# Optimization experiments

Hardware: AMD Instinct MI355X
Metric: run time of the kernel (lower is better)

## Reference

```python
import jax, jax.numpy as jnp
import numpy as np

NUM_EXECUTORS = 50
NUM_DAG_FEATURES = 3
EMB_DAG = 16
EMB_GLOB = 16
HIDDEN = [64, 64, 32]
B = 60000            # number of jobs (one per env in the batched rollout)
NODES_PER_JOB = 10
NODE_FEAT = 5


def _init_mlp(key, dims):
    ws, bs = [], []
    for i in range(len(dims) - 1):
        key, k = jax.random.split(key)
        scale = 1.0 / np.sqrt(dims[i])
        ws.append(jax.random.uniform(k, (dims[i], dims[i + 1]), jnp.float32, -scale, scale))
        bs.append(jnp.zeros((dims[i + 1],), jnp.float32))
    return ws, bs


def setup_inputs() -> dict:
    rng = np.random.default_rng(0)
    n_nodes = B * NODES_PER_JOB
    # dag_batch.ptr: job i owns nodes [i*NODES_PER_JOB, (i+1)*NODES_PER_JOB)
    ptr = np.arange(B + 1, dtype=np.int64) * NODES_PER_JOB
    job_indices = rng.permutation(B).astype(np.int64)
    # ragged action counts per job (exec_mask is a prefix mask of length num_exec_acts[i])
    num_exec_acts = rng.integers(1, NUM_EXECUTORS + 1, size=B).astype(np.int64)
    n_sel = num_exec_acts[job_indices]
    T = int(n_sel.sum())
    # per-ragged-row executor index: concat([arange(n) for n in n_sel]), vectorized
    starts = np.cumsum(n_sel) - n_sel
    exec_act_idx = (np.arange(T, dtype=np.int64) - np.repeat(starts, n_sel)).astype(np.int64)

    key = jax.random.key(0)
    k_x, k_hd, k_hg, k_mlp = jax.random.split(key, 4)
    x = jax.random.normal(k_x, (n_nodes, NODE_FEAT), jnp.float32)
    h_dag = jax.random.normal(k_hd, (B, EMB_DAG), jnp.float32)
    h_glob = jax.random.normal(k_hg, (B, EMB_GLOB), jnp.float32)

    in_dim = NUM_DAG_FEATURES + EMB_DAG + EMB_GLOB + 1  # 36
    ws, bs = _init_mlp(k_mlp, [in_dim] + HIDDEN + [1])

    return {
        "x": x,
        "h_dag": h_dag,
        "h_glob": h_glob,
        "ptr": jnp.asarray(ptr),
        "job_indices": jnp.asarray(job_indices),
        "num_exec_acts": jnp.asarray(num_exec_acts),
        "exec_act_idx": jnp.asarray(exec_act_idx),
        "W1": ws[0], "b1": bs[0],
        "W2": ws[1], "b2": bs[1],
        "W3": ws[2], "b3": bs[2],
        "W4": ws[3], "b4": bs[3],
    }


def reference(x, h_dag, h_glob, ptr, job_indices, num_exec_acts, exec_act_idx,
              W1, b1, W2, b2, W3, b3, W4, b4):
    T = exec_act_idx.shape[0]                       # total ragged action rows (static)
    J = job_indices.shape[0]
    # masked gather: dag features at each dag's start node, then select jobs
    x_dag = x[ptr[:-1], :NUM_DAG_FEATURES][job_indices]        # [J, 3]
    h_dag_sel = h_dag[job_indices]                              # [J, 16]
    x_h_dag = jnp.concatenate([x_dag, h_dag_sel], axis=1)       # [J, 19]
    # variable repeat_interleave -> gather by repeated row index
    n_sel = num_exec_acts[job_indices]
    rpt = jnp.repeat(jnp.arange(J), n_sel, total_repeat_length=T)
    x_h_rpt = x_h_dag[rpt]                                      # [T, 19]
    h_glob_rpt = h_glob[rpt]                                    # [T, 16]
    # exec action feature: k / num_executors for the k-th valid executor
    exec_actions = (exec_act_idx.astype(x.dtype) / NUM_EXECUTORS)[:, None]  # [T, 1]
    h = jnp.concatenate([x_h_rpt, h_glob_rpt, exec_actions], axis=1)        # [T, 36]
    h = jax.nn.relu(h @ W1 + b1)
    h = jax.nn.relu(h @ W2 + b2)
    h = jax.nn.relu(h @ W3 + b3)
    scores = (h @ W4 + b4).squeeze(-1)                          # [T]
    return scores
```

## Files before the change

kernel.cpp:

```cpp
#include <hip/hip_runtime.h>

#define TPB 256

using half8  = __attribute__((ext_vector_type(8))) _Float16;
using fp16x2 = __attribute__((ext_vector_type(2))) __fp16;
using f32x4  = __attribute__((ext_vector_type(4))) float;

static __device__ __forceinline__ unsigned short h2u(_Float16 h) {
    union { _Float16 h; unsigned short u; } v; v.h = h; return v.u;
}
static __device__ __forceinline__ unsigned pkrtz(float a, float b) {
    fp16x2 h = __builtin_amdgcn_cvt_pkrtz(a, b);
    return __builtin_bit_cast(unsigned, h);
}
template <int CTRL>
static __device__ __forceinline__ float dppmov(float x) {
    return __int_as_float(__builtin_amdgcn_mov_dpp(__float_as_int(x), CTRL, 0xF, 0xF, true));
}
#define DPP_SWAP 0xB1

__global__ __launch_bounds__(TPB) void k_prep(const float* __restrict__ x,
                                              const float* __restrict__ h_dag,
                                              const float* __restrict__ h_glob,
                                              const int* __restrict__ ptr,
                                              const int* __restrict__ job_indices,
                                              const int* __restrict__ num_exec_acts,
                                              int J, int nb,
                                              unsigned int* __restrict__ feat,
                                              int* __restrict__ bsum, int* __restrict__ jsv,
                                              const float* __restrict__ W1,
                                              const float* __restrict__ b1,
                                              const float* __restrict__ W2,
                                              const float* __restrict__ b2,
                                              const float* __restrict__ W3,
                                              const float* __restrict__ b3,
                                              const float* __restrict__ W4,
                                              uint4* __restrict__ wfrag,
                                              float4* __restrict__ bfrag)
{
    if (blockIdx.x == (unsigned)nb) {
        if (threadIdx.x < 64) {
            int lane = threadIdx.x;
            int n = lane & 15, q = lane >> 4;
#pragma unroll
            for (int nt = 0; nt < 4; nt++) {
#pragma unroll
                for (int s = 0; s < 2; s++) {
                    half8 w1f, w2f;
#pragma unroll
                    for (int jj = 0; jj < 8; jj++) {
                        int ks = s * 32 + q * 8 + jj;
                        w1f[jj] = (ks < 36) ? (_Float16)W1[ks * 64 + nt * 16 + n] : (_Float16)0.0f;
                        w2f[jj] = (_Float16)W2[ks * 64 + nt * 16 + n];
                    }
                    wfrag[(nt * 2 + s) * 64 + lane]     = __builtin_bit_cast(uint4, w1f);
                    wfrag[(8 + nt * 2 + s) * 64 + lane] = __builtin_bit_cast(uint4, w2f);
                }
            }
#pragma unroll
            for (int nt = 0; nt < 2; nt++) {
#pragma unroll
                for (int s = 0; s < 2; s++) {
                    half8 w3f;
#pragma unroll
                    for (int jj = 0; jj < 8; jj++) {
                        int ks = s * 32 + q * 8 + jj;
                        w3f[jj] = (_Float16)W3[ks * 32 + nt * 16 + n];
                    }
                    wfrag[(16 + nt * 2 + s) * 64 + lane] = __builtin_bit_cast(uint4, w3f);
                }
            }
            bfrag[0 * 64 + lane] = make_float4(b1[n], b1[16 + n], b1[32 + n], b1[48 + n]);
            bfrag[1 * 64 + lane] = make_float4(b2[n], b2[16 + n], b2[32 + n], b2[48 + n]);
            bfrag[2 * 64 + lane] = make_float4(b3[n], b3[16 + n], W4[n], W4[16 + n]);
        }
        return;
    }

    __shared__ int sc[TPB];
    int j = blockIdx.x * TPB + threadIdx.x;
    int v = 0;
    if (j < J) {
        int ji   = job_indices[j];
        v        = num_exec_acts[ji];
        int node = ptr[ji];
        float f[40];
        f[0] = x[node * 5 + 0];
        f[1] = x[node * 5 + 1];
        f[2] = x[node * 5 + 2];
        float4 hd[4], hg[4];
#pragma unroll
        for (int c4 = 0; c4 < 4; c4++) hd[c4] = *(const float4*)(h_dag + (size_t)ji * 16 + 4 * c4);
#pragma unroll
        for (int c4 = 0; c4 < 4; c4++) hg[c4] = *(const float4*)(h_glob + (size_t)j * 16 + 4 * c4);
#pragma unroll
        for (int c4 = 0; c4 < 4; c4++) {
            f[3 + 4 * c4 + 0]  = hd[c4].x; f[3 + 4 * c4 + 1]  = hd[c4].y;
            f[3 + 4 * c4 + 2]  = hd[c4].z; f[3 + 4 * c4 + 3]  = hd[c4].w;
            f[19 + 4 * c4 + 0] = hg[c4].x; f[19 + 4 * c4 + 1] = hg[c4].y;
            f[19 + 4 * c4 + 2] = hg[c4].z; f[19 + 4 * c4 + 3] = hg[c4].w;
        }
#pragma unroll
        for (int c = 35; c < 40; c++) f[c] = 0.0f;
        unsigned int w[20];
#pragma unroll
        for (int k = 0; k < 20; k++)
            w[k] = (unsigned)h2u((_Float16)f[2 * k]) | ((unsigned)h2u((_Float16)f[2 * k + 1]) << 16);
        uint4* dst = (uint4*)(feat + (size_t)j * 20);
#pragma unroll
        for (int qq = 0; qq < 5; qq++)
            dst[qq] = make_uint4(w[4 * qq], w[4 * qq + 1], w[4 * qq + 2], w[4 * qq + 3]);
    }
    sc[threadIdx.x] = v;
    __syncthreads();
    for (int d = 1; d < TPB; d <<= 1) {
        int add = (threadIdx.x >= d) ? sc[threadIdx.x - d] : 0;
        __syncthreads();
        sc[threadIdx.x] += add;
        __syncthreads();
    }
    if (j < J) jsv[j] = ((sc[threadIdx.x] - v) << 6) | v;
    if (threadIdx.x == TPB - 1) bsum[blockIdx.x] = sc[TPB - 1];
}

__global__ __launch_bounds__(TPB) void k_mlp_mfma(const unsigned int* __restrict__ feat,
                                                  const int* __restrict__ jsv,
                                                  const int* __restrict__ bsum,
                                                  const uint4* __restrict__ wfrag,
                                                  const float4* __restrict__ bfrag,
                                                  const float* __restrict__ b4,
                                                  float* __restrict__ out,
                                                  int T, int J, int nb, int numTiles, int chunk)
{
    __shared__ __align__(16) char smem[4 * 4096];
    __shared__ int boffs[TPB];
    __shared__ int swin[4][64];
    __shared__ int srow[4][64];
    const int tid  = threadIdx.x;
    const int lane = tid & 63;
    const int wv   = tid >> 6;
    const int n    = lane & 15;
    const int q    = lane >> 4;
    char* slab = smem + wv * 4096;

    {
        int v = (tid < nb) ? bsum[tid] : 0;
        boffs[tid] = v;
        __syncthreads();
        for (int d = 1; d < TPB; d <<= 1) {
            int add = (tid >= d) ? boffs[tid - d] : 0;
            __syncthreads();
            boffs[tid] += add;
            __syncthreads();
        }
        int ex = boffs[tid] - v;
        __syncthreads();
        boffs[tid] = ex;
        __syncthreads();
    }

    half8 bw1[4][2], bw2[4][2], bw3[2][2];
#pragma unroll
    for (int nt = 0; nt < 4; nt++)
#pragma unroll
        for (int s = 0; s < 2; s++) {
            bw1[nt][s] = __builtin_bit_cast(half8, wfrag[(nt * 2 + s) * 64 + lane]);
            bw2[nt][s] = __builtin_bit_cast(half8, wfrag[(8 + nt * 2 + s) * 64 + lane]);
        }
#pragma unroll
    for (int nt = 0; nt < 2; nt++)
#pragma unroll
        for (int s = 0; s < 2; s++)
            bw3[nt][s] = __builtin_bit_cast(half8, wfrag[(16 + nt * 2 + s) * 64 + lane]);

    float4 bf1 = bfrag[0 * 64 + lane];
    float4 bf2 = bfrag[1 * 64 + lane];
    float4 bf3 = bfrag[2 * 64 + lane];
    float bb1[4] = {bf1.x, bf1.y, bf1.z, bf1.w};
    float bb2[4] = {bf2.x, bf2.y, bf2.z, bf2.w};
    float bb3[2] = {bf3.x, bf3.y};
    const float w4a = bf3.z, w4b = bf3.w;
    const float b4v = b4[0];
    const int   swr = (n >> 1) & 7;
    const int   odd = n & 1;

    const int t0 = blockIdx.x * chunk;
    const int t1 = (t0 + chunk < numTiles) ? (t0 + chunk) : numTiles;
    const int R  = (t1 - t0) * 32;
    const int r0 = t0 * 128 + wv * R;
    int rend = r0 + R;
    if (rend > T) rend = T;

    if (r0 < rend) {
        int j_lo;
        {
            int lo = 0, hi = nb - 1;
            while (lo < hi) {
                int mid = (lo + hi + 1) >> 1;
                if (boffs[mid] <= r0) lo = mid; else hi = mid - 1;
            }
            j_lo = lo << 8;
        }
        int sreg    = 0;
        int win_top = 0x80000000;

        half8 a1[4][2];
        auto body32 = [&](int rbb, int ab) {
#pragma unroll
            for (int mt = 0; mt < 2; mt++) {
                f32x4 acc[4];
#pragma unroll
                for (int nt = 0; nt < 4; nt++) { f32x4 c; c[0]=c[1]=c[2]=c[3]=bb1[nt]; acc[nt]=c; }
#pragma unroll
                for (int s = 0; s < 2; s++) {
#pragma unroll
                    for (int nt = 0; nt < 4; nt++)
                        acc[nt] = __builtin_amdgcn_mfma_f32_16x16x32_f16(a1[ab + mt][s], bw1[nt][s], acc[nt], 0, 0, 0);
                }
                unsigned* sl = (unsigned*)slab;
#pragma unroll
                for (int nt = 0; nt < 4; nt++) {
                    float v0 = fmaxf(acc[nt][0], 0.0f), v1 = fmaxf(acc[nt][1], 0.0f);
                    float v2 = fmaxf(acc[nt][2], 0.0f), v3 = fmaxf(acc[nt][3], 0.0f);
                    float t0_ = dppmov<DPP_SWAP>(v0), t1_ = dppmov<DPP_SWAP>(v1);
                    float t2_ = dppmov<DPP_SWAP>(v2), t3_ = dppmov<DPP_SWAP>(v3);
                    unsigned u0 = pkrtz(odd ? t2_ : v0, odd ? v2 : t0_);
                    unsigned u1 = pkrtz(odd ? t3_ : v1, odd ? v3 : t1_);
                    int rowA = 16 * mt + 4 * q + (odd ? 2 : 0);
                    int c    = 2 * nt + (n >> 3);
                    int a0   = (rowA * 8 + (c ^ ((rowA >> 1) & 7))) * 4 + ((n >> 1) & 3);
                    sl[a0] = u0; sl[a0 + 32] = u1;
                }
            }

#pragma unroll
            for (int mt = 0; mt < 2; mt++) {
                const int M0 = 16 * mt;
                f32x4 acc[4];
#pragma unroll
                for (int nt = 0; nt < 4; nt++) { f32x4 c; c[0]=c[1]=c[2]=c[3]=bb2[nt]; acc[nt]=c; }
#pragma unroll
                for (int s = 0; s < 2; s++) {
                    half8 a = *(const half8*)(slab + ((M0 + n) * 8 + ((s * 4 + q) ^ swr)) * 16);
#pragma unroll
                    for (int nt = 0; nt < 4; nt++)
                        acc[nt] = __builtin_amdgcn_mfma_f32_16x16x32_f16(a, bw2[nt][s], acc[nt], 0, 0, 0);
                }
                unsigned* sl = (unsigned*)slab;
#pragma unroll
                for (int nt = 0; nt < 4; nt++) {
                    float v0 = fmaxf(acc[nt][0], 0.0f), v1 = fmaxf(acc[nt][1], 0.0f);
                    float v2 = fmaxf(acc[nt][2], 0.0f), v3 = fmaxf(acc[nt][3], 0.0f);
                    float t0_ = dppmov<DPP_SWAP>(v0), t1_ = dppmov<DPP_SWAP>(v1);
                    float t2_ = dppmov<DPP_SWAP>(v2), t3_ = dppmov<DPP_SWAP>(v3);
                    unsigned u0 = pkrtz(odd ? t2_ : v0, odd ? v2 : t0_);
                    unsigned u1 = pkrtz(odd ? t3_ : v1, odd ? v3 : t1_);
                    int rowA = M0 + 4 * q + (odd ? 2 : 0);
                    int c    = 2 * nt + (n >> 3);
                    int a0   = (rowA * 8 + (c ^ ((rowA >> 1) & 7))) * 4 + ((n >> 1) & 3);
                    sl[a0] = u0; sl[a0 + 32] = u1;
                }
            }

#pragma unroll
            for (int mt = 0; mt < 2; mt++) {
                const int M0 = 16 * mt;
                f32x4 acc[2];
#pragma unroll
                for (int nt = 0; nt < 2; nt++) { f32x4 c; c[0]=c[1]=c[2]=c[3]=bb3[nt]; acc[nt]=c; }
#pragma unroll
                for (int s = 0; s < 2; s++) {
                    half8 a = *(const half8*)(slab + ((M0 + n) * 8 + ((s * 4 + q) ^ swr)) * 16);
#pragma unroll
                    for (int nt = 0; nt < 2; nt++)
                        acc[nt] = __builtin_amdgcn_mfma_f32_16x16x32_f16(a, bw3[nt][s], acc[nt], 0, 0, 0);
                }
                f32x4 red;
#pragma unroll
                for (int r = 0; r < 4; r++)
                    red[r] = fmaxf(acc[0][r], 0.0f) * w4a + fmaxf(acc[1][r], 0.0f) * w4b;
#pragma unroll
                for (int r = 0; r < 4; r++) {
                    red[r] += dppmov<0x121>(red[r]);
                    red[r] += dppmov<0x122>(red[r]);
                    red[r] += dppmov<0x124>(red[r]);
                    red[r] += dppmov<0x128>(red[r]);
                }
                int t = rbb + M0 + q * 4 + n;
                float val = (n == 0) ? red[0] : (n == 1) ? red[1] : (n == 2) ? red[2] : red[3];
                if (n < 4 && t < T) out[t] = val + b4v;
            }
        };

        for (int rb = r0; rb < rend; rb += 64) {
            if (win_top <= rb + 63) {
                for (;;) {
                    int jj = j_lo + lane;
                    sreg = (jj < J) ? (boffs[jj >> 8] + (jsv[jj] >> 6)) : 0x7fffffff;
                    unsigned long long m = __ballot(sreg <= rb);
                    int adv = 63 - __builtin_clzll(m);
                    j_lo += adv;
                    if (adv == 0) break;
                }
                swin[wv][lane] = sreg;
                win_top = __shfl(sreg, 63);
            }

            {
                int rt = rb + lane;
                const int* sw = swin[wv];
                int lj = 0;
#pragma unroll
                for (int stp = 32; stp; stp >>= 1) {
                    int c2 = lj + stp;
                    if (c2 < 64 && sw[c2] <= rt) lj = c2;
                }
                srow[wv][lane] = (lj << 8) | (rt - sw[lj]);
            }

#pragma unroll
            for (int mt = 0; mt < 4; mt++) {
                int  rt    = rb + 16 * mt + n;
                bool valid = rt < T;
                int  u     = srow[wv][16 * mt + n];
                int  jj2   = j_lo + (u >> 8);
                const uint4* fsrc = (const uint4*)(feat + (size_t)jj2 * 20);
                uint4 g0 = fsrc[q];
                a1[mt][0] = __builtin_bit_cast(half8, g0);
                uint4 g1 = make_uint4(0, 0, 0, 0);
                if (q == 0) {
                    g1 = fsrc[4];
                    float fe = valid ? (float)(u & 255) * 0.02f : 0.0f;
                    g1.y = (g1.y & 0xffffu) | ((unsigned)h2u((_Float16)fe) << 16);
                }
                a1[mt][1] = __builtin_bit_cast(half8, g1);
            }

            body32(rb, 0);
            if (rb + 32 < rend) body32(rb + 32, 2);
        }
    }
}

extern "C" void kernel_launch(void* const* d_in, const int* in_sizes, int n_in,
                              void* d_out, int out_size, void* d_ws, size_t ws_size,
                              hipStream_t stream)
{
    const float* x             = (const float*)d_in[0];
    const float* h_dag         = (const float*)d_in[1];
    const float* h_glob        = (const float*)d_in[2];
    const int*   ptr           = (const int*)d_in[3];
    const int*   job_indices   = (const int*)d_in[4];
    const int*   num_exec_acts = (const int*)d_in[5];
    const float* W1 = (const float*)d_in[7];
    const float* b1 = (const float*)d_in[8];
    const float* W2 = (const float*)d_in[9];
    const float* b2 = (const float*)d_in[10];
    const float* W3 = (const float*)d_in[11];
    const float* b3 = (const float*)d_in[12];
    const float* W4 = (const float*)d_in[13];
    const float* b4 = (const float*)d_in[14];
    float* out = (float*)d_out;

    int J  = in_sizes[4];
    int T  = in_sizes[6];
    int nb = (J + TPB - 1) / TPB;

    char* wsp = (char*)d_ws;
    int* bsum = (int*)wsp;
    wsp += (((size_t)nb * 4) + 255) / 256 * 256;
    int* jsv = (int*)wsp;
    wsp += (((size_t)J * 4) + 255) / 256 * 256;
    uint4* wfrag = (uint4*)wsp;
    wsp += 20 * 64 * 16;
    float4* bfrag = (float4*)wsp;
    wsp += 3 * 64 * 16;
    unsigned int* feat = (unsigned int*)wsp;

    k_prep<<<nb + 1, TPB, 0, stream>>>(x, h_dag, h_glob, ptr, job_indices, num_exec_acts,
                                       J, nb, feat, bsum, jsv,
                                       W1, b1, W2, b2, W3, b3, W4, wfrag, bfrag);

    int numTiles = (T + 127) / 128;
    int grid = numTiles < 1280 ? numTiles : 1280;
    int chunk = (numTiles + grid - 1) / grid;
    grid = (numTiles + chunk - 1) / chunk;
    k_mlp_mfma<<<grid, TPB, 0, stream>>>(feat, jsv, bsum, wfrag, bfrag, b4,
                                         out, T, J, nb, numTiles, chunk);
}
```

Measured before the change: 180.2 us.

## Precompute per-job first-layer preactivations and drop the layer-1 MFMA per row

Layer 1 is linear in the 35 per-job features, so the prep kernel now computes the full 64-wide layer-1 preactivation (bias included) once per job in fp32 and stores it in a per-job table. The MLP kernel adds only the rank-1 term from the executor feature, applies relu, and packs the result to fp16 as the layer-2 MFMA input. This removes the layer-1 MFMA work, its LDS round trip and the feature packing for every ragged row. In exchange the per-job table grows from 80 to 256 bytes, each row gathers more bytes, and the prep kernel does about 2240 FMAs per job with uniform weight loads.

```diff
diff --git a/kernel.cpp b/kernel.cpp
--- a/kernel.cpp
+++ b/kernel.cpp
@@ -6,9 +6,6 @@
 using fp16x2 = __attribute__((ext_vector_type(2))) __fp16;
 using f32x4  = __attribute__((ext_vector_type(4))) float;
 
-static __device__ __forceinline__ unsigned short h2u(_Float16 h) {
-    union { _Float16 h; unsigned short u; } v; v.h = h; return v.u;
-}
 static __device__ __forceinline__ unsigned pkrtz(float a, float b) {
     fp16x2 h = __builtin_amdgcn_cvt_pkrtz(a, b);
     return __builtin_bit_cast(unsigned, h);
@@ -26,7 +23,7 @@
                                               const int* __restrict__ job_indices,
                                               const int* __restrict__ num_exec_acts,
                                               int J, int nb,
-                                              unsigned int* __restrict__ feat,
+                                              float* __restrict__ s_tab,
                                               int* __restrict__ bsum, int* __restrict__ jsv,
                                               const float* __restrict__ W1,
                                               const float* __restrict__ b1,
@@ -46,14 +43,12 @@
             for (int nt = 0; nt < 4; nt++) {
 #pragma unroll
                 for (int s = 0; s < 2; s++) {
-                    half8 w1f, w2f;
+                    half8 w2f;
 #pragma unroll
                     for (int jj = 0; jj < 8; jj++) {
                         int ks = s * 32 + q * 8 + jj;
-                        w1f[jj] = (ks < 36) ? (_Float16)W1[ks * 64 + nt * 16 + n] : (_Float16)0.0f;
                         w2f[jj] = (_Float16)W2[ks * 64 + nt * 16 + n];
                     }
-                    wfrag[(nt * 2 + s) * 64 + lane]     = __builtin_bit_cast(uint4, w1f);
                     wfrag[(8 + nt * 2 + s) * 64 + lane] = __builtin_bit_cast(uint4, w2f);
                 }
             }
@@ -70,7 +65,6 @@
                     wfrag[(16 + nt * 2 + s) * 64 + lane] = __builtin_bit_cast(uint4, w3f);
                 }
             }
-            bfrag[0 * 64 + lane] = make_float4(b1[n], b1[16 + n], b1[32 + n], b1[48 + n]);
             bfrag[1 * 64 + lane] = make_float4(b2[n], b2[16 + n], b2[32 + n], b2[48 + n]);
             bfrag[2 * 64 + lane] = make_float4(b3[n], b3[16 + n], W4[n], W4[16 + n]);
         }
@@ -84,7 +78,7 @@
         int ji   = job_indices[j];
         v        = num_exec_acts[ji];
         int node = ptr[ji];
-        float f[40];
+        float f[35];
         f[0] = x[node * 5 + 0];
         f[1] = x[node * 5 + 1];
         f[2] = x[node * 5 + 2];
@@ -100,16 +94,27 @@
             f[19 + 4 * c4 + 0] = hg[c4].x; f[19 + 4 * c4 + 1] = hg[c4].y;
             f[19 + 4 * c4 + 2] = hg[c4].z; f[19 + 4 * c4 + 3] = hg[c4].w;
         }
-#pragma unroll
-        for (int c = 35; c < 40; c++) f[c] = 0.0f;
-        unsigned int w[20];
-#pragma unroll
-        for (int k = 0; k < 20; k++)
-            w[k] = (unsigned)h2u((_Float16)f[2 * k]) | ((unsigned)h2u((_Float16)f[2 * k + 1]) << 16);
-        uint4* dst = (uint4*)(feat + (size_t)j * 20);
-#pragma unroll
-        for (int qq = 0; qq < 5; qq++)
-            dst[qq] = make_uint4(w[4 * qq], w[4 * qq + 1], w[4 * qq + 2], w[4 * qq + 3]);
+        float acc[64];
+#pragma unroll
+        for (int d4 = 0; d4 < 16; d4++) {
+            float4 b = *(const float4*)(b1 + 4 * d4);
+            acc[4 * d4 + 0] = b.x; acc[4 * d4 + 1] = b.y;
+            acc[4 * d4 + 2] = b.z; acc[4 * d4 + 3] = b.w;
+        }
+#pragma unroll
+        for (int c = 0; c < 35; c++) {
+            float fc = f[c];
+#pragma unroll
+            for (int d4 = 0; d4 < 16; d4++) {
+                float4 w = *(const float4*)(W1 + c * 64 + 4 * d4);
+                acc[4 * d4 + 0] += fc * w.x; acc[4 * d4 + 1] += fc * w.y;
+                acc[4 * d4 + 2] += fc * w.z; acc[4 * d4 + 3] += fc * w.w;
+            }
+        }
+        float4* sd = (float4*)(s_tab + (size_t)j * 64);
+#pragma unroll
+        for (int d4 = 0; d4 < 16; d4++)
+            sd[d4] = make_float4(acc[4 * d4], acc[4 * d4 + 1], acc[4 * d4 + 2], acc[4 * d4 + 3]);
     }
     sc[threadIdx.x] = v;
     __syncthreads();
@@ -123,7 +128,8 @@
     if (threadIdx.x == TPB - 1) bsum[blockIdx.x] = sc[TPB - 1];
 }
 
-__global__ __launch_bounds__(TPB) void k_mlp_mfma(const unsigned int* __restrict__ feat,
+__global__ __launch_bounds__(TPB) void k_mlp_mfma(const float* __restrict__ s_tab,
+                                                  const float* __restrict__ W1,
                                                   const int* __restrict__ jsv,
                                                   const int* __restrict__ bsum,
                                                   const uint4* __restrict__ wfrag,
@@ -159,30 +165,39 @@
         __syncthreads();
     }
 
-    half8 bw1[4][2], bw2[4][2], bw3[2][2];
+    half8 bw2[4][2], bw3[2][2];
 #pragma unroll
     for (int nt = 0; nt < 4; nt++)
 #pragma unroll
-        for (int s = 0; s < 2; s++) {
-            bw1[nt][s] = __builtin_bit_cast(half8, wfrag[(nt * 2 + s) * 64 + lane]);
+        for (int s = 0; s < 2; s++)
             bw2[nt][s] = __builtin_bit_cast(half8, wfrag[(8 + nt * 2 + s) * 64 + lane]);
-        }
 #pragma unroll
     for (int nt = 0; nt < 2; nt++)
 #pragma unroll
         for (int s = 0; s < 2; s++)
             bw3[nt][s] = __builtin_bit_cast(half8, wfrag[(16 + nt * 2 + s) * 64 + lane]);
 
-    float4 bf1 = bfrag[0 * 64 + lane];
     float4 bf2 = bfrag[1 * 64 + lane];
     float4 bf3 = bfrag[2 * 64 + lane];
-    float bb1[4] = {bf1.x, bf1.y, bf1.z, bf1.w};
     float bb2[4] = {bf2.x, bf2.y, bf2.z, bf2.w};
     float bb3[2] = {bf3.x, bf3.y};
     const float w4a = bf3.z, w4b = bf3.w;
     const float b4v = b4[0];
     const int   swr = (n >> 1) & 7;
     const int   odd = n & 1;
+
+    float w36[16];
+    {
+        const float* wp = W1 + 35 * 64 + q * 8;
+        float4 wa0 = *(const float4*)(wp);
+        float4 wa1 = *(const float4*)(wp + 4);
+        float4 wb0 = *(const float4*)(wp + 32);
+        float4 wb1 = *(const float4*)(wp + 36);
+        w36[0]=wa0.x; w36[1]=wa0.y; w36[2]=wa0.z; w36[3]=wa0.w;
+        w36[4]=wa1.x; w36[5]=wa1.y; w36[6]=wa1.z; w36[7]=wa1.w;
+        w36[8]=wb0.x; w36[9]=wb0.y; w36[10]=wb0.z; w36[11]=wb0.w;
+        w36[12]=wb1.x; w36[13]=wb1.y; w36[14]=wb1.z; w36[15]=wb1.w;
+    }
 
     const int t0 = blockIdx.x * chunk;
     const int t1 = (t0 + chunk < numTiles) ? (t0 + chunk) : numTiles;
@@ -204,18 +219,47 @@
         int sreg    = 0;
         int win_top = 0x80000000;
 
-        half8 a1[4][2];
-        auto body32 = [&](int rbb, int ab) {
+        half8 a2[2][2];
+
+        auto build_a2 = [&](int mtbase) {
+#pragma unroll
+            for (int m = 0; m < 2; m++) {
+                int u   = srow[wv][16 * (mtbase + m) + n];
+                int job = j_lo + (u >> 8);
+                if (job > J - 1) job = J - 1;
+                float e = (float)(u & 255) * 0.02f;
+                const float* sp = s_tab + (size_t)job * 64 + q * 8;
+                float4 s0 = *(const float4*)(sp);
+                float4 s1 = *(const float4*)(sp + 4);
+                float4 s2 = *(const float4*)(sp + 32);
+                float4 s3 = *(const float4*)(sp + 36);
+                float h[16];
+                h[0]  = fmaxf(s0.x + e * w36[0],  0.0f); h[1]  = fmaxf(s0.y + e * w36[1],  0.0f);
+                h[2]  = fmaxf(s0.z + e * w36[2],  0.0f); h[3]  = fmaxf(s0.w + e * w36[3],  0.0f);
+                h[4]  = fmaxf(s1.x + e * w36[4],  0.0f); h[5]  = fmaxf(s1.y + e * w36[5],  0.0f);
+                h[6]  = fmaxf(s1.z + e * w36[6],  0.0f); h[7]  = fmaxf(s1.w + e * w36[7],  0.0f);
+                h[8]  = fmaxf(s2.x + e * w36[8],  0.0f); h[9]  = fmaxf(s2.y + e * w36[9],  0.0f);
+                h[10] = fmaxf(s2.z + e * w36[10], 0.0f); h[11] = fmaxf(s2.w + e * w36[11], 0.0f);
+                h[12] = fmaxf(s3.x + e * w36[12], 0.0f); h[13] = fmaxf(s3.y + e * w36[13], 0.0f);
+                h[14] = fmaxf(s3.z + e * w36[14], 0.0f); h[15] = fmaxf(s3.w + e * w36[15], 0.0f);
+                a2[m][0] = __builtin_bit_cast(half8, make_uint4(pkrtz(h[0], h[1]),  pkrtz(h[2], h[3]),
+                                                                pkrtz(h[4], h[5]),  pkrtz(h[6], h[7])));
+                a2[m][1] = __builtin_bit_cast(half8, make_uint4(pkrtz(h[8], h[9]),  pkrtz(h[10], h[11]),
+                                                                pkrtz(h[12], h[13]), pkrtz(h[14], h[15])));
+            }
+        };
+
+        auto stage_L2r = [&]() {
 #pragma unroll
             for (int mt = 0; mt < 2; mt++) {
                 f32x4 acc[4];
 #pragma unroll
-                for (int nt = 0; nt < 4; nt++) { f32x4 c; c[0]=c[1]=c[2]=c[3]=bb1[nt]; acc[nt]=c; }
+                for (int nt = 0; nt < 4; nt++) { f32x4 c; c[0]=c[1]=c[2]=c[3]=bb2[nt]; acc[nt]=c; }
 #pragma unroll
                 for (int s = 0; s < 2; s++) {
 #pragma unroll
                     for (int nt = 0; nt < 4; nt++)
-                        acc[nt] = __builtin_amdgcn_mfma_f32_16x16x32_f16(a1[ab + mt][s], bw1[nt][s], acc[nt], 0, 0, 0);
+                        acc[nt] = __builtin_amdgcn_mfma_f32_16x16x32_f16(a2[mt][s], bw2[nt][s], acc[nt], 0, 0, 0);
                 }
                 unsigned* sl = (unsigned*)slab;
 #pragma unroll
@@ -232,36 +276,9 @@
                     sl[a0] = u0; sl[a0 + 32] = u1;
                 }
             }
-
-#pragma unroll
-            for (int mt = 0; mt < 2; mt++) {
-                const int M0 = 16 * mt;
-                f32x4 acc[4];
-#pragma unroll
-                for (int nt = 0; nt < 4; nt++) { f32x4 c; c[0]=c[1]=c[2]=c[3]=bb2[nt]; acc[nt]=c; }
-#pragma unroll
-                for (int s = 0; s < 2; s++) {
-                    half8 a = *(const half8*)(slab + ((M0 + n) * 8 + ((s * 4 + q) ^ swr)) * 16);
-#pragma unroll
-                    for (int nt = 0; nt < 4; nt++)
-                        acc[nt] = __builtin_amdgcn_mfma_f32_16x16x32_f16(a, bw2[nt][s], acc[nt], 0, 0, 0);
-                }
-                unsigned* sl = (unsigned*)slab;
-#pragma unroll
-                for (int nt = 0; nt < 4; nt++) {
-                    float v0 = fmaxf(acc[nt][0], 0.0f), v1 = fmaxf(acc[nt][1], 0.0f);
-                    float v2 = fmaxf(acc[nt][2], 0.0f), v3 = fmaxf(acc[nt][3], 0.0f);
-                    float t0_ = dppmov<DPP_SWAP>(v0), t1_ = dppmov<DPP_SWAP>(v1);
-                    float t2_ = dppmov<DPP_SWAP>(v2), t3_ = dppmov<DPP_SWAP>(v3);
-                    unsigned u0 = pkrtz(odd ? t2_ : v0, odd ? v2 : t0_);
-                    unsigned u1 = pkrtz(odd ? t3_ : v1, odd ? v3 : t1_);
-                    int rowA = M0 + 4 * q + (odd ? 2 : 0);
-                    int c    = 2 * nt + (n >> 3);
-                    int a0   = (rowA * 8 + (c ^ ((rowA >> 1) & 7))) * 4 + ((n >> 1) & 3);
-                    sl[a0] = u0; sl[a0 + 32] = u1;
-                }
-            }
-
+        };
+
+        auto stage_L34 = [&](int rbb) {
 #pragma unroll
             for (int mt = 0; mt < 2; mt++) {
                 const int M0 = 16 * mt;
@@ -318,26 +335,14 @@
                 srow[wv][lane] = (lj << 8) | (rt - sw[lj]);
             }
 
-#pragma unroll
-            for (int mt = 0; mt < 4; mt++) {
-                int  rt    = rb + 16 * mt + n;
-                bool valid = rt < T;
-                int  u     = srow[wv][16 * mt + n];
-                int  jj2   = j_lo + (u >> 8);
-                const uint4* fsrc = (const uint4*)(feat + (size_t)jj2 * 20);
-                uint4 g0 = fsrc[q];
-                a1[mt][0] = __builtin_bit_cast(half8, g0);
-                uint4 g1 = make_uint4(0, 0, 0, 0);
-                if (q == 0) {
-                    g1 = fsrc[4];
-                    float fe = valid ? (float)(u & 255) * 0.02f : 0.0f;
-                    g1.y = (g1.y & 0xffffu) | ((unsigned)h2u((_Float16)fe) << 16);
-                }
-                a1[mt][1] = __builtin_bit_cast(half8, g1);
-            }
-
-            body32(rb, 0);
-            if (rb + 32 < rend) body32(rb + 32, 2);
+            build_a2(0);
+            stage_L2r();
+            stage_L34(rb);
+            if (rb + 32 < rend) {
+                build_a2(2);
+                stage_L2r();
+                stage_L34(rb + 32);
+            }
         }
     }
 }
@@ -375,16 +380,16 @@
     wsp += 20 * 64 * 16;
     float4* bfrag = (float4*)wsp;
     wsp += 3 * 64 * 16;
-    unsigned int* feat = (unsigned int*)wsp;
+    float* s_tab = (float*)wsp;
 
     k_prep<<<nb + 1, TPB, 0, stream>>>(x, h_dag, h_glob, ptr, job_indices, num_exec_acts,
-                                       J, nb, feat, bsum, jsv,
+                                       J, nb, s_tab, bsum, jsv,
                                        W1, b1, W2, b2, W3, b3, W4, wfrag, bfrag);
 
     int numTiles = (T + 127) / 128;
     int grid = numTiles < 1280 ? numTiles : 1280;
     int chunk = (numTiles + grid - 1) / grid;
     grid = (numTiles + chunk - 1) / chunk;
-    k_mlp_mfma<<<grid, TPB, 0, stream>>>(feat, jsv, bsum, wfrag, bfrag, b4,
+    k_mlp_mfma<<<grid, TPB, 0, stream>>>(s_tab, W1, jsv, bsum, wfrag, bfrag, b4,
                                          out, T, J, nb, numTiles, chunk);
 }
```

Result: faster. 171.7 us (-4.7%).
